# Kernel tuning notes

Measured on AMD Instinct MI355X. Metric: run time of the kernel, lower is better.

The kernel has to match this reference:

```python
import jax, jax.numpy as jnp
import numpy as np

EMBED_DIM = 384

def setup_inputs() -> dict:
    key = jax.random.key(0)
    k1, k2, k3 = jax.random.split(key, 3)
    B, P, N, d = 8, 4, 4096, EMBED_DIM
    hidden_states = jax.random.normal(k1, (B, P, N, d), dtype=jnp.float32)
    # 1x1 conv == pointwise linear over channel dim; scale like fan-in init
    w_qkv = jax.random.normal(k2, (d, 1 + 2 * d), dtype=jnp.float32) * (1.0 / np.sqrt(d))
    b_qkv = jnp.zeros((1 + 2 * d,), dtype=jnp.float32)
    w_out = jax.random.normal(k3, (d, d), dtype=jnp.float32) * (1.0 / np.sqrt(d))
    b_out = jnp.zeros((d,), dtype=jnp.float32)
    return {"hidden_states": hidden_states, "w_qkv": w_qkv, "b_qkv": b_qkv,
            "w_out": w_out, "b_out": b_out}

def reference(hidden_states, w_qkv, b_qkv, w_out, b_out):
    d = EMBED_DIM
    # qkv 1x1 conv (channels-last): [B,P,N,d] @ [d, 1+2d]
    qkv = jnp.einsum("bpnd,de->bpne", hidden_states, w_qkv) + b_qkv
    query = qkv[..., :1]                # [B,P,N,1]
    key_ = qkv[..., 1:1 + d]            # [B,P,N,d]
    value = qkv[..., 1 + d:]            # [B,P,N,d]
    # softmax over token axis (axis=2); attn_dropout=0.0 -> identity
    context_scores = jax.nn.softmax(query, axis=2)
    # softmax-weighted pooling of keys over tokens -> [B,P,1,d]
    context_vector = jnp.sum(key_ * context_scores, axis=2, keepdims=True)
    # relu-gated broadcast multiply
    out = context_vector * jax.nn.relu(value)
    # out 1x1 conv
    out = jnp.einsum("bpnd,de->bpne", out, w_out) + b_out
    return out
```

## Files before the change

### kernel.cpp

```cpp
#include <hip/hip_runtime.h>

#define D     384
#define E     769
#define NTOK  4096
#define BPN   32
#define NCH   64

typedef short s16x8 __attribute__((ext_vector_type(8)));
typedef float f32x4 __attribute__((ext_vector_type(4)));
typedef float f32x2 __attribute__((ext_vector_type(2)));

__device__ __forceinline__ unsigned short f2bf(float f){
  unsigned int u = __builtin_bit_cast(unsigned int, f);
  u += 0x7FFFu + ((u >> 16) & 1u);
  return (unsigned short)(u >> 16);
}

__global__ void k0_prep(const float* __restrict__ wqkv, const float* __restrict__ wout,
                        float* __restrict__ wq, unsigned short* __restrict__ wvF,
                        unsigned short* __restrict__ woF){
  int tid = blockIdx.x*256 + threadIdx.x;
  if (tid < D) wq[tid] = wqkv[(size_t)tid*E];
  if (tid < 24*12*64*8){
    int pos = tid & 7;
    int lane = (tid >> 3) & 63;
    int kt  = (tid >> 9) % 12;
    int nt  = tid / 6144;
    int l15 = lane & 15, l4 = lane >> 4;
    int col = nt*16 + l15;
    int k   = kt*32 + l4*8 + pos;
    wvF[tid] = f2bf(wqkv[(size_t)k*E + 385 + col]);
    woF[tid] = f2bf(wout[(size_t)k*D + col]);
  }
}

__global__ __launch_bounds__(512)
void kA_fused(const float* __restrict__ H, const float* __restrict__ wq,
              float* __restrict__ partial, float* __restrict__ mArr,
              float* __restrict__ lArr){
  __shared__ float red[8][392];
  __shared__ float qs[32];
  __shared__ float ws[32];
  __shared__ float scaleS;
  const int ch = blockIdx.x, bp = blockIdx.y;
  const int t = threadIdx.x, w = t >> 6, lane = t & 63;
  const size_t base0 = (size_t)bp*NTOK + (size_t)ch*64;

  f32x2 wqr[3];
  #pragma unroll
  for (int seg=0;seg<3;++seg)
    wqr[seg] = *reinterpret_cast<const f32x2*>(wq + lane*2 + seg*128);

  float acc6[6] = {0.f,0.f,0.f,0.f,0.f,0.f};
  float mRun = -3.4e38f, lRun = 0.f;

  #pragma unroll 1
  for (int s=0; s<2; ++s){
    f32x2 h[4][3];
    #pragma unroll
    for (int j=0;j<4;++j){
      const float* hr = H + (base0 + (size_t)(s*32 + w*4 + j))*D + lane*2;
      #pragma unroll
      for (int seg=0;seg<3;++seg)
        h[j][seg] = *reinterpret_cast<const f32x2*>(hr + seg*128);
    }
    float a[4];
    #pragma unroll
    for (int j=0;j<4;++j)
      a[j] = h[j][0].x*wqr[0].x + h[j][0].y*wqr[0].y
           + h[j][1].x*wqr[1].x + h[j][1].y*wqr[1].y
           + h[j][2].x*wqr[2].x + h[j][2].y*wqr[2].y;
    #pragma unroll
    for (int off=32; off; off>>=1){
      #pragma unroll
      for (int j=0;j<4;++j) a[j] += __shfl_xor(a[j], off, 64);
    }
    if (lane == 0){
      qs[w*4+0]=a[0]; qs[w*4+1]=a[1]; qs[w*4+2]=a[2]; qs[w*4+3]=a[3];
    }
    __syncthreads();

    if (w == 0){
      float q = (lane < 32) ? qs[lane] : -3.4e38f;
      float msub = q;
      #pragma unroll
      for (int off=32; off; off>>=1) msub = fmaxf(msub, __shfl_xor(msub, off, 64));
      float mNew = fmaxf(mRun, msub);
      float sc   = __expf(mRun - mNew);
      float e    = (lane < 32) ? __expf(q - mNew) : 0.f;
      if (lane < 32) ws[lane] = e;
      float lsub = e;
      #pragma unroll
      for (int off=32; off; off>>=1) lsub += __shfl_xor(lsub, off, 64);
      lRun = lRun*sc + lsub;
      mRun = mNew;
      if (lane == 0) scaleS = sc;
    }
    __syncthreads();

    float sc  = scaleS;
    float wj0 = ws[w*4+0], wj1 = ws[w*4+1], wj2 = ws[w*4+2], wj3 = ws[w*4+3];
    #pragma unroll
    for (int seg=0;seg<3;++seg){
      acc6[seg*2]   = acc6[seg*2]*sc
                    + wj0*h[0][seg].x + wj1*h[1][seg].x
                    + wj2*h[2][seg].x + wj3*h[3][seg].x;
      acc6[seg*2+1] = acc6[seg*2+1]*sc
                    + wj0*h[0][seg].y + wj1*h[1][seg].y
                    + wj2*h[2][seg].y + wj3*h[3][seg].y;
    }
  }

  #pragma unroll
  for (int seg=0;seg<3;++seg){
    red[w][lane*2+seg*128]   = acc6[seg*2];
    red[w][lane*2+seg*128+1] = acc6[seg*2+1];
  }
  __syncthreads();
  if (t < D){
    float s8 = 0.f;
    #pragma unroll
    for (int w8=0;w8<8;++w8) s8 += red[w8][t];
    partial[((size_t)bp*NCH + ch)*D + t] = s8;
  }
  if (t == 0){ mArr[bp*NCH + ch] = mRun; lArr[bp*NCH + ch] = lRun; }
}

__global__ void kB_cv(const float* __restrict__ partial, const float* __restrict__ mArr,
                      const float* __restrict__ lArr, const float* __restrict__ wqkv,
                      const float* __restrict__ bqkv, float* __restrict__ cv){
  __shared__ float S[D];
  const int bp = blockIdx.x, t = threadIdx.x;
  float M = -3.4e38f;
  #pragma unroll 4
  for (int c = 0; c < NCH; ++c) M = fmaxf(M, mArr[bp*NCH + c]);
  float num = 0.f, den = 0.f;
  #pragma unroll 2
  for (int c = 0; c < NCH; ++c){
    float f = __expf(mArr[bp*NCH + c] - M);
    num += f * partial[((size_t)bp*NCH + c)*D + t];
    den += f * lArr[bp*NCH + c];
  }
  S[t] = num / den;
  __syncthreads();
  float acc = bqkv[1 + t];
  #pragma unroll 4
  for (int k = 0; k < D; ++k)
    acc += S[k] * wqkv[(size_t)k*E + 1 + t];
  cv[(size_t)bp*D + t] = acc;
}

#define BM 64
#define LOADW(W, kt, n) (*reinterpret_cast<const s16x8*>(&(W)[((size_t)((n)*12+(kt))*64 + lane)*8]))

__global__ __launch_bounds__(512, 2)
void k5_main(const float* __restrict__ H, const unsigned short* __restrict__ wvF,
             const unsigned short* __restrict__ woF, const float* __restrict__ cv,
             const float* __restrict__ bqkv, const float* __restrict__ bout,
             float* __restrict__ out){
  __shared__ unsigned short As[BM*D];
  const int bp = blockIdx.y;
  const int m0 = blockIdx.x*BM;
  const size_t rowbase = (size_t)bp*NTOK + m0;
  const float* A = H + rowbase*D;
  const int t = threadIdx.x;
  const int wave = t>>6, lane = t&63;
  const int l15 = lane&15, l4 = lane>>4;
  const int n0 = wave*48;
  const unsigned short* wvW = wvF + (size_t)wave*3*12*512;
  const unsigned short* woW = woF + (size_t)wave*3*12*512;

  #pragma unroll
  for (int i=0;i<12;++i){
    int c = t + i*512;
    int idx8 = c >> 1;
    int l15v = idx8 & 15;
    int l4v  = (idx8 >> 4) & 3;
    int ktv  = (idx8 >> 6) % 12;
    int mv   = idx8 / 768;
    f32x4 v = *reinterpret_cast<const f32x4*>(
        A + (size_t)(mv*16 + l15v)*D + ktv*32 + l4v*8 + (c&1)*4);
    ushort4 b;
    b.x=f2bf(v.x); b.y=f2bf(v.y); b.z=f2bf(v.z); b.w=f2bf(v.w);
    *reinterpret_cast<ushort4*>(&As[c*4]) = b;
  }

  s16x8 b0[3], b1[3];
  #pragma unroll
  for (int n=0;n<3;++n) b0[n] = LOADW(wvW, 0, n);
  #pragma unroll
  for (int n=0;n<3;++n) b1[n] = LOADW(wvW, 1, n);
  __syncthreads();

  f32x4 acc[4][3] = {};
  #pragma unroll
  for (int kt=0; kt<12; ++kt){
    s16x8 bp_[3];
    if (kt < 10){
      #pragma unroll
      for (int n=0;n<3;++n) bp_[n] = LOADW(wvW, kt+2, n);
    }
    s16x8 a[4];
    #pragma unroll
    for (int m=0;m<4;++m)
      a[m] = *reinterpret_cast<const s16x8*>(&As[((m*12+kt)*64 + lane)*8]);
    #pragma unroll
    for (int m=0;m<4;++m)
      #pragma unroll
      for (int n=0;n<3;++n)
        acc[m][n] = __builtin_amdgcn_mfma_f32_16x16x32_bf16(a[m], b0[n], acc[m][n], 0,0,0);
    #pragma unroll
    for (int n=0;n<3;++n){ b0[n] = b1[n]; b1[n] = bp_[n]; }
  }

  float bv[3], cvv[3];
  #pragma unroll
  for (int n=0;n<3;++n){
    int col = n0 + n*16 + l15;
    bv[n]  = bqkv[385+col];
    cvv[n] = cv[(size_t)bp*D + col];
  }
  #pragma unroll
  for (int n=0;n<3;++n) b0[n] = LOADW(woW, 0, n);
  #pragma unroll
  for (int n=0;n<3;++n) b1[n] = LOADW(woW, 1, n);
  __syncthreads();

  #pragma unroll
  for (int n=0;n<3;++n){
    int col  = n0 + n*16 + l15;
    int kt2  = col >> 5;
    int l42  = (col >> 3) & 3;
    int pos2 = col & 7;
    #pragma unroll
    for (int m=0;m<4;++m){
      #pragma unroll
      for (int r=0;r<4;++r){
        int row = l4*4 + r;
        float v = acc[m][n][r] + bv[n];
        v = v > 0.f ? v*cvv[n] : 0.f;
        As[((m*12+kt2)*64 + l42*16 + row)*8 + pos2] = f2bf(v);
      }
    }
  }
  #pragma unroll
  for (int m=0;m<4;++m)
    #pragma unroll
    for (int n=0;n<3;++n)
      acc[m][n] = (f32x4){0.f,0.f,0.f,0.f};
  __syncthreads();

  #pragma unroll
  for (int kt=0; kt<12; ++kt){
    s16x8 bp_[3];
    if (kt < 10){
      #pragma unroll
      for (int n=0;n<3;++n) bp_[n] = LOADW(woW, kt+2, n);
    }
    s16x8 a[4];
    #pragma unroll
    for (int m=0;m<4;++m)
      a[m] = *reinterpret_cast<const s16x8*>(&As[((m*12+kt)*64 + lane)*8]);
    #pragma unroll
    for (int m=0;m<4;++m)
      #pragma unroll
      for (int n=0;n<3;++n)
        acc[m][n] = __builtin_amdgcn_mfma_f32_16x16x32_bf16(a[m], b0[n], acc[m][n], 0,0,0);
    #pragma unroll
    for (int n=0;n<3;++n){ b0[n] = b1[n]; b1[n] = bp_[n]; }
  }

  #pragma unroll
  for (int n=0;n<3;++n){
    int col = n0 + n*16 + l15;
    float bo = bout[col];
    #pragma unroll
    for (int m=0;m<4;++m)
      #pragma unroll
      for (int r=0;r<4;++r){
        int row = m*16 + l4*4 + r;
        out[(rowbase+row)*D + col] = acc[m][n][r] + bo;
      }
  }
}

extern "C" void kernel_launch(void* const* d_in, const int* in_sizes, int n_in,
                              void* d_out, int out_size, void* d_ws, size_t ws_size,
                              hipStream_t stream){
  const float* H    = (const float*)d_in[0];
  const float* wqkv = (const float*)d_in[1];
  const float* bqkv = (const float*)d_in[2];
  const float* wout = (const float*)d_in[3];
  const float* bout = (const float*)d_in[4];
  float* out = (float*)d_out;

  char* ws = (char*)d_ws;
  float*          partial = (float*)(ws + 0x000000);
  float*          mArr    = (float*)(ws + 0x300000);
  float*          lArr    = (float*)(ws + 0x302000);
  float*          cv      = (float*)(ws + 0x304000);
  float*          wq      = (float*)(ws + 0x310000);
  unsigned short* wvF     = (unsigned short*)(ws + 0x311000);
  unsigned short* woF     = (unsigned short*)(ws + 0x359000);

  hipLaunchKernelGGL(k0_prep,  dim3(576),          dim3(256), 0, stream, wqkv, wout, wq, wvF, woF);
  hipLaunchKernelGGL(kA_fused, dim3(NCH, BPN),     dim3(512), 0, stream, H, wq, partial, mArr, lArr);
  hipLaunchKernelGGL(kB_cv,    dim3(BPN),          dim3(384), 0, stream, partial, mArr, lArr, wqkv, bqkv, cv);
  hipLaunchKernelGGL(k5_main,  dim3(NTOK/BM, BPN), dim3(512), 0, stream, H, wvF, woF, cv, bqkv, bout, out);
}
```

Before: 221.2 us.

## Process two row tiles per block, prefetching the second tile's inputs into registers

Each k5_main block now handles two consecutive 64-row tiles instead of one, which halves the grid. While the first tile's two GEMMs run, the second tile's fp32 activations are already loaded into registers (inflB), so global load latency is hidden behind MFMA work. The cost is 48 extra VGPRs of prefetch state under launch_bounds(512,2), which may cause spills or lower occupancy, and fewer blocks to spread across the CUs.

```diff
diff --git a/kernel.cpp b/kernel.cpp
--- a/kernel.cpp
+++ b/kernel.cpp
@@ -160,9 +160,7 @@
              float* __restrict__ out){
   __shared__ unsigned short As[BM*D];
   const int bp = blockIdx.y;
-  const int m0 = blockIdx.x*BM;
-  const size_t rowbase = (size_t)bp*NTOK + m0;
-  const float* A = H + rowbase*D;
+  const int g0 = blockIdx.x*2;
   const int t = threadIdx.x;
   const int wave = t>>6, lane = t&63;
   const int l15 = lane&15, l4 = lane>>4;
@@ -170,6 +168,7 @@
   const unsigned short* wvW = wvF + (size_t)wave*3*12*512;
   const unsigned short* woW = woF + (size_t)wave*3*12*512;
 
+  int offs[12];
   #pragma unroll
   for (int i=0;i<12;++i){
     int c = t + i*512;
@@ -178,21 +177,44 @@
     int l4v  = (idx8 >> 4) & 3;
     int ktv  = (idx8 >> 6) % 12;
     int mv   = idx8 / 768;
-    f32x4 v = *reinterpret_cast<const f32x4*>(
-        A + (size_t)(mv*16 + l15v)*D + ktv*32 + l4v*8 + (c&1)*4);
+    offs[i] = (mv*16 + l15v)*D + ktv*32 + l4v*8 + (c&1)*4;
+  }
+
+  const size_t rowbase0 = (size_t)bp*NTOK + (size_t)g0*BM;
+  const float* A0 = H + rowbase0*D;
+  const float* A1 = A0 + (size_t)BM*D;
+
+  f32x4 inflA[12];
+  #pragma unroll
+  for (int i=0;i<12;++i)
+    inflA[i] = *reinterpret_cast<const f32x4*>(A0 + offs[i]);
+
+  float bv[3], cvv[3];
+  s16x8 b0[3], b1[3];
+  f32x4 acc[4][3];
+  f32x4 inflB[12];
+
+  #pragma unroll
+  for (int i=0;i<12;++i){
+    int c = t + i*512;
     ushort4 b;
-    b.x=f2bf(v.x); b.y=f2bf(v.y); b.z=f2bf(v.z); b.w=f2bf(v.w);
+    b.x=f2bf(inflA[i].x); b.y=f2bf(inflA[i].y); b.z=f2bf(inflA[i].z); b.w=f2bf(inflA[i].w);
     *reinterpret_cast<ushort4*>(&As[c*4]) = b;
   }
-
-  s16x8 b0[3], b1[3];
+  #pragma unroll
+  for (int i=0;i<12;++i)
+    inflB[i] = *reinterpret_cast<const f32x4*>(A1 + offs[i]);
   #pragma unroll
   for (int n=0;n<3;++n) b0[n] = LOADW(wvW, 0, n);
   #pragma unroll
   for (int n=0;n<3;++n) b1[n] = LOADW(wvW, 1, n);
   __syncthreads();
 
-  f32x4 acc[4][3] = {};
+  #pragma unroll
+  for (int m=0;m<4;++m)
+    #pragma unroll
+    for (int n=0;n<3;++n)
+      acc[m][n] = (f32x4){0.f,0.f,0.f,0.f};
   #pragma unroll
   for (int kt=0; kt<12; ++kt){
     s16x8 bp_[3];
@@ -212,8 +234,6 @@
     #pragma unroll
     for (int n=0;n<3;++n){ b0[n] = b1[n]; b1[n] = bp_[n]; }
   }
-
-  float bv[3], cvv[3];
   #pragma unroll
   for (int n=0;n<3;++n){
     int col = n0 + n*16 + l15;
@@ -269,7 +289,6 @@
     #pragma unroll
     for (int n=0;n<3;++n){ b0[n] = b1[n]; b1[n] = bp_[n]; }
   }
-
   #pragma unroll
   for (int n=0;n<3;++n){
     int col = n0 + n*16 + l15;
@@ -279,8 +298,111 @@
       #pragma unroll
       for (int r=0;r<4;++r){
         int row = m*16 + l4*4 + r;
-        out[(rowbase+row)*D + col] = acc[m][n][r] + bo;
+        out[(rowbase0+row)*D + col] = acc[m][n][r] + bo;
       }
+  }
+
+  __syncthreads();
+  #pragma unroll
+  for (int i=0;i<12;++i){
+    int c = t + i*512;
+    ushort4 b;
+    b.x=f2bf(inflB[i].x); b.y=f2bf(inflB[i].y); b.z=f2bf(inflB[i].z); b.w=f2bf(inflB[i].w);
+    *reinterpret_cast<ushort4*>(&As[c*4]) = b;
+  }
+  #pragma unroll
+  for (int n=0;n<3;++n) b0[n] = LOADW(wvW, 0, n);
+  #pragma unroll
+  for (int n=0;n<3;++n) b1[n] = LOADW(wvW, 1, n);
+  __syncthreads();
+
+  #pragma unroll
+  for (int m=0;m<4;++m)
+    #pragma unroll
+    for (int n=0;n<3;++n)
+      acc[m][n] = (f32x4){0.f,0.f,0.f,0.f};
+  #pragma unroll
+  for (int kt=0; kt<12; ++kt){
+    s16x8 bp_[3];
+    if (kt < 10){
+      #pragma unroll
+      for (int n=0;n<3;++n) bp_[n] = LOADW(wvW, kt+2, n);
+    }
+    s16x8 a[4];
+    #pragma unroll
+    for (int m=0;m<4;++m)
+      a[m] = *reinterpret_cast<const s16x8*>(&As[((m*12+kt)*64 + lane)*8]);
+    #pragma unroll
+    for (int m=0;m<4;++m)
+      #pragma unroll
+      for (int n=0;n<3;++n)
+        acc[m][n] = __builtin_amdgcn_mfma_f32_16x16x32_bf16(a[m], b0[n], acc[m][n], 0,0,0);
+    #pragma unroll
+    for (int n=0;n<3;++n){ b0[n] = b1[n]; b1[n] = bp_[n]; }
+  }
+  #pragma unroll
+  for (int n=0;n<3;++n) b0[n] = LOADW(woW, 0, n);
+  #pragma unroll
+  for (int n=0;n<3;++n) b1[n] = LOADW(woW, 1, n);
+  __syncthreads();
+
+  #pragma unroll
+  for (int n=0;n<3;++n){
+    int col  = n0 + n*16 + l15;
+    int kt2  = col >> 5;
+    int l42  = (col >> 3) & 3;
+    int pos2 = col & 7;
+    #pragma unroll
+    for (int m=0;m<4;++m){
+      #pragma unroll
+      for (int r=0;r<4;++r){
+        int row = l4*4 + r;
+        float v = acc[m][n][r] + bv[n];
+        v = v > 0.f ? v*cvv[n] : 0.f;
+        As[((m*12+kt2)*64 + l42*16 + row)*8 + pos2] = f2bf(v);
+      }
+    }
+  }
+  #pragma unroll
+  for (int m=0;m<4;++m)
+    #pragma unroll
+    for (int n=0;n<3;++n)
+      acc[m][n] = (f32x4){0.f,0.f,0.f,0.f};
+  __syncthreads();
+
+  #pragma unroll
+  for (int kt=0; kt<12; ++kt){
+    s16x8 bp_[3];
+    if (kt < 10){
+      #pragma unroll
+      for (int n=0;n<3;++n) bp_[n] = LOADW(woW, kt+2, n);
+    }
+    s16x8 a[4];
+    #pragma unroll
+    for (int m=0;m<4;++m)
+      a[m] = *reinterpret_cast<const s16x8*>(&As[((m*12+kt)*64 + lane)*8]);
+    #pragma unroll
+    for (int m=0;m<4;++m)
+      #pragma unroll
+      for (int n=0;n<3;++n)
+        acc[m][n] = __builtin_amdgcn_mfma_f32_16x16x32_bf16(a[m], b0[n], acc[m][n], 0,0,0);
+    #pragma unroll
+    for (int n=0;n<3;++n){ b0[n] = b1[n]; b1[n] = bp_[n]; }
+  }
+  {
+    const size_t rowbase1 = rowbase0 + BM;
+    #pragma unroll
+    for (int n=0;n<3;++n){
+      int col = n0 + n*16 + l15;
+      float bo = bout[col];
+      #pragma unroll
+      for (int m=0;m<4;++m)
+        #pragma unroll
+        for (int r=0;r<4;++r){
+          int row = m*16 + l4*4 + r;
+          out[(rowbase1+row)*D + col] = acc[m][n][r] + bo;
+        }
+    }
   }
 }
 
@@ -303,8 +425,8 @@
   unsigned short* wvF     = (unsigned short*)(ws + 0x311000);
   unsigned short* woF     = (unsigned short*)(ws + 0x359000);
 
-  hipLaunchKernelGGL(k0_prep,  dim3(576),          dim3(256), 0, stream, wqkv, wout, wq, wvF, woF);
-  hipLaunchKernelGGL(kA_fused, dim3(NCH, BPN),     dim3(512), 0, stream, H, wq, partial, mArr, lArr);
-  hipLaunchKernelGGL(kB_cv,    dim3(BPN),          dim3(384), 0, stream, partial, mArr, lArr, wqkv, bqkv, cv);
-  hipLaunchKernelGGL(k5_main,  dim3(NTOK/BM, BPN), dim3(512), 0, stream, H, wvF, woF, cv, bqkv, bout, out);
-}
+  hipLaunchKernelGGL(k0_prep,  dim3(576),              dim3(256), 0, stream, wqkv, wout, wq, wvF, woF);
+  hipLaunchKernelGGL(kA_fused, dim3(NCH, BPN),         dim3(512), 0, stream, H, wq, partial, mArr, lArr);
+  hipLaunchKernelGGL(kB_cv,    dim3(BPN),              dim3(384), 0, stream, partial, mArr, lArr, wqkv, bqkv, cv);
+  hipLaunchKernelGGL(k5_main,  dim3(NTOK/(BM*2), BPN), dim3(512), 0, stream, H, wvF, woF, cv, bqkv, bout, out);
+}
```

Measured after the change: 248.4 us. +12.3%, slower.
